# Optimization experiments

Measured on AMD Instinct MI355X. Metric: run time of the kernel, lower is better.

The kernel has to match this reference:

```python
import jax, jax.numpy as jnp
import numpy as np

B, N, M = 128, 256, 1024
EPS = 1e-16
NORM_EPS = 1e-8  # torch cosine_similarity denominator clamp


def setup_inputs() -> dict:
    key = jax.random.key(0)
    ks = jax.random.split(key, 9)
    return {
        "memory": jax.random.normal(ks[0], (B, N, M), jnp.float32),
        "k": jax.random.normal(ks[1], (B, M), jnp.float32),
        "beta": jax.random.uniform(ks[2], (B, 1), jnp.float32),
        "g": jax.random.uniform(ks[3], (B, 1), jnp.float32),
        "s": jax.random.uniform(ks[4], (B, 3), jnp.float32),
        "gamma": jax.random.uniform(ks[5], (B, 1), jnp.float32),
        "w_prev": jax.random.uniform(ks[6], (B, N), jnp.float32),
        "e": jax.random.uniform(ks[7], (B, M), jnp.float32),
        "a": jax.random.normal(ks[8], (B, M), jnp.float32),
    }


def reference(memory, k, beta, g, s, gamma, w_prev, e, a):
    # --- _similarity: cosine similarity + softmax over N rows ---
    mem_e = memory + EPS              # (B, N, M)
    k_e = k + EPS                     # (B, M)
    dot = jnp.einsum("bnm,bm->bn", mem_e, k_e)
    mnorm = jnp.maximum(jnp.linalg.norm(mem_e, axis=-1), NORM_EPS)      # (B, N)
    knorm = jnp.maximum(jnp.linalg.norm(k_e, axis=-1), NORM_EPS)        # (B,)
    cos = dot / (mnorm * knorm[:, None])
    w_c = jax.nn.softmax(beta * cos, axis=-1)                           # (B, N)

    # --- _interpolate with previous weighting ---
    w_g = g * w_c + (1.0 - g) * w_prev                                  # (B, N)

    # --- _shift: circular convolution with 3-tap kernel s ---
    # result[m] = s0*w[m-1] + s1*w[m] + s2*w[m+1]  (circular, matches _convolve)
    w_t = (s[:, 0:1] * jnp.roll(w_g, 1, axis=1)
           + s[:, 1:2] * w_g
           + s[:, 2:3] * jnp.roll(w_g, -1, axis=1))                     # (B, N)

    # --- _sharpen ---
    w_pow = w_t ** gamma
    w = w_pow / (jnp.sum(w_pow, axis=1, keepdims=True) + EPS)           # (B, N)

    # --- write: batched outer-product erase/add (fused, no per-batch loop) ---
    erase = jnp.einsum("bn,bm->bnm", w, e)                              # (B, N, M)
    add = jnp.einsum("bn,bm->bnm", w, a)                                # (B, N, M)
    new_memory = memory * (1.0 - erase) + add

    # --- read ---
    read = jnp.einsum("bn,bnm->bm", w, new_memory)                      # (B, M)

    return read, new_memory, w
```

## Files before the change

kernel.cpp:

```cpp
#include <hip/hip_runtime.h>

#define B_ 128
#define N_ 256
#define M_ 1024
#define EPS_ 1e-16f
#define NORM_EPS_ 1e-8f

#define SPLIT_ 8
#define NSUB_ (N_ / SPLIT_)

typedef float f32x4 __attribute__((ext_vector_type(4)));

__device__ __forceinline__ float wave_reduce_sum(float v) {
#pragma unroll
    for (int off = 32; off; off >>= 1) v += __shfl_xor(v, off, 64);
    return v;
}

__device__ __forceinline__ float wave_reduce_max(float v) {
#pragma unroll
    for (int off = 32; off; off >>= 1) v = fmaxf(v, __shfl_xor(v, off, 64));
    return v;
}

__global__ void sim_kernel(const float* __restrict__ memory,
                           const float* __restrict__ k,
                           float* __restrict__ dot_out,
                           float* __restrict__ mnorm2_out,
                           float* __restrict__ read_out) {
    const int wave = threadIdx.x >> 6;
    const int lane = threadIdx.x & 63;
    const int row  = blockIdx.x * 4 + wave;
    const int b    = row >> 8;

    if (blockIdx.x < (B_ * M_) / 256) {
        read_out[blockIdx.x * 256 + threadIdx.x] = 0.f;
    }

    const f32x4* __restrict__ mrow = (const f32x4*)(memory + (size_t)row * M_);
    const f32x4* __restrict__ krow = (const f32x4*)(k + (size_t)b * M_);

    float dacc = 0.f, nacc = 0.f;
#pragma unroll
    for (int it = 0; it < 4; ++it) {
        const int idx = it * 64 + lane;
        f32x4 mv = mrow[idx];
        f32x4 kv = krow[idx];
        float m0 = mv.x + EPS_, m1 = mv.y + EPS_, m2 = mv.z + EPS_, m3 = mv.w + EPS_;
        float c0 = kv.x + EPS_, c1 = kv.y + EPS_, c2 = kv.z + EPS_, c3 = kv.w + EPS_;
        dacc += m0 * c0 + m1 * c1 + m2 * c2 + m3 * c3;
        nacc += m0 * m0 + m1 * m1 + m2 * m2 + m3 * m3;
    }
    dacc = wave_reduce_sum(dacc);
    nacc = wave_reduce_sum(nacc);
    if (lane == 0) {
        dot_out[row]    = dacc;
        mnorm2_out[row] = nacc;
    }
}

__global__ void fused_weight_write_kernel(const float* __restrict__ memory,
                                          const float* __restrict__ k,
                                          const float* __restrict__ beta,
                                          const float* __restrict__ g,
                                          const float* __restrict__ s,
                                          const float* __restrict__ gamma,
                                          const float* __restrict__ w_prev,
                                          const float* __restrict__ e,
                                          const float* __restrict__ a,
                                          const float* __restrict__ dot_in,
                                          const float* __restrict__ mnorm2_in,
                                          float* __restrict__ w_out,
                                          float* __restrict__ newmem_out,
                                          float* __restrict__ read_out) {
    const int b    = blockIdx.x >> 3;
    const int part = blockIdx.x & (SPLIT_ - 1);
    const int tid  = threadIdx.x;
    const int lane = tid & 63;
    const int wave = tid >> 6;
    const int n    = tid;

    __shared__ float red[4];
    __shared__ float s_wg[N_];

    f32x4 kv = ((const f32x4*)(k + (size_t)b * M_))[tid];
    float k0 = kv.x + EPS_, k1 = kv.y + EPS_, k2 = kv.z + EPS_, k3 = kv.w + EPS_;
    float kk = k0 * k0 + k1 * k1 + k2 * k2 + k3 * k3;
    kk = wave_reduce_sum(kk);
    if (lane == 0) red[wave] = kk;
    __syncthreads();
    const float knorm = fmaxf(sqrtf(red[0] + red[1] + red[2] + red[3]), NORM_EPS_);
    __syncthreads();

    const float mnorm = fmaxf(sqrtf(mnorm2_in[(size_t)b * N_ + n]), NORM_EPS_);
    const float cosv  = dot_in[(size_t)b * N_ + n] / (mnorm * knorm);
    const float x     = beta[b] * cosv;

    float mx = wave_reduce_max(x);
    if (lane == 0) red[wave] = mx;
    __syncthreads();
    mx = fmaxf(fmaxf(red[0], red[1]), fmaxf(red[2], red[3]));
    __syncthreads();
    const float ex = __expf(x - mx);
    float es = wave_reduce_sum(ex);
    if (lane == 0) red[wave] = es;
    __syncthreads();
    es = red[0] + red[1] + red[2] + red[3];
    __syncthreads();
    const float w_c = ex / es;

    const float gb  = g[b];
    const float w_g = gb * w_c + (1.f - gb) * w_prev[(size_t)b * N_ + n];
    s_wg[n] = w_g;
    __syncthreads();

    const float s0 = s[b * 3 + 0], s1 = s[b * 3 + 1], s2 = s[b * 3 + 2];
    const float w_t = s0 * s_wg[(n + N_ - 1) & (N_ - 1)]
                    + s1 * s_wg[n]
                    + s2 * s_wg[(n + 1) & (N_ - 1)];
    __syncthreads();

    const float w_pow = powf(w_t, gamma[b]);
    float ps = wave_reduce_sum(w_pow);
    if (lane == 0) red[wave] = ps;
    __syncthreads();
    ps = red[0] + red[1] + red[2] + red[3];
    const float w_final = w_pow / (ps + EPS_);

    s_wg[n] = w_final;
    if (part == 0) w_out[(size_t)b * N_ + n] = w_final;
    __syncthreads();

    const f32x4 ev = ((const f32x4*)(e + (size_t)b * M_))[tid];
    const f32x4 av = ((const f32x4*)(a + (size_t)b * M_))[tid];

    const size_t base = (size_t)b * N_ * M_;
    f32x4 racc = {0.f, 0.f, 0.f, 0.f};

#pragma unroll 4
    for (int j = 0; j < NSUB_; ++j) {
        const int nn = part * NSUB_ + j;
        const f32x4 mv = ((const f32x4*)(memory + base + (size_t)nn * M_))[tid];
        const float wn = s_wg[part * NSUB_ + j];
        f32x4 nv;
        nv.x = mv.x * (1.f - wn * ev.x) + wn * av.x;
        nv.y = mv.y * (1.f - wn * ev.y) + wn * av.y;
        nv.z = mv.z * (1.f - wn * ev.z) + wn * av.z;
        nv.w = mv.w * (1.f - wn * ev.w) + wn * av.w;
        ((f32x4*)(newmem_out + base + (size_t)nn * M_))[tid] = nv;
        racc.x += wn * nv.x;
        racc.y += wn * nv.y;
        racc.z += wn * nv.z;
        racc.w += wn * nv.w;
    }

    float* rrow = read_out + (size_t)b * M_ + tid * 4;
    atomicAdd(rrow + 0, racc.x);
    atomicAdd(rrow + 1, racc.y);
    atomicAdd(rrow + 2, racc.z);
    atomicAdd(rrow + 3, racc.w);
}

extern "C" void kernel_launch(void* const* d_in, const int* in_sizes, int n_in,
                              void* d_out, int out_size, void* d_ws, size_t ws_size,
                              hipStream_t stream) {
    (void)in_sizes; (void)n_in; (void)out_size; (void)ws_size;

    const float* memory = (const float*)d_in[0];
    const float* k      = (const float*)d_in[1];
    const float* beta   = (const float*)d_in[2];
    const float* g      = (const float*)d_in[3];
    const float* s      = (const float*)d_in[4];
    const float* gamma  = (const float*)d_in[5];
    const float* w_prev = (const float*)d_in[6];
    const float* e      = (const float*)d_in[7];
    const float* a      = (const float*)d_in[8];

    float* out        = (float*)d_out;
    float* read_out   = out;
    float* newmem_out = out + (size_t)B_ * M_;
    float* w_out      = newmem_out + (size_t)B_ * N_ * M_;

    float* ws        = (float*)d_ws;
    float* dot_ws    = ws;
    float* mnorm2_ws = ws + (size_t)B_ * N_;

    sim_kernel<<<(B_ * N_) / 4, 256, 0, stream>>>(memory, k, dot_ws, mnorm2_ws,
                                                  read_out);
    fused_weight_write_kernel<<<B_ * SPLIT_, 256, 0, stream>>>(
        memory, k, beta, g, s, gamma, w_prev, e, a,
        dot_ws, mnorm2_ws, w_out, newmem_out, read_out);
}
```

Measured before the change: 270.9 us.

## Double write-kernel split and batch sixteen rows per similarity block

```diff
diff --git a/kernel.cpp b/kernel.cpp
--- a/kernel.cpp
+++ b/kernel.cpp
@@ -6,8 +6,9 @@
 #define EPS_ 1e-16f
 #define NORM_EPS_ 1e-8f
 
-#define SPLIT_ 8
+#define SPLIT_ 16
 #define NSUB_ (N_ / SPLIT_)
+#define SIMROWS_ 16
 
 typedef float f32x4 __attribute__((ext_vector_type(4)));
 
@@ -30,32 +31,41 @@
                            float* __restrict__ read_out) {
     const int wave = threadIdx.x >> 6;
     const int lane = threadIdx.x & 63;
-    const int row  = blockIdx.x * 4 + wave;
-    const int b    = row >> 8;
-
-    if (blockIdx.x < (B_ * M_) / 256) {
-        read_out[blockIdx.x * 256 + threadIdx.x] = 0.f;
+    const int blk  = blockIdx.x;
+    const int b    = blk >> 4;
+
+    if (blk < (B_ * M_) / 256) {
+        read_out[blk * 256 + threadIdx.x] = 0.f;
     }
 
-    const f32x4* __restrict__ mrow = (const f32x4*)(memory + (size_t)row * M_);
     const f32x4* __restrict__ krow = (const f32x4*)(k + (size_t)b * M_);
-
-    float dacc = 0.f, nacc = 0.f;
+    const f32x4 kv0 = krow[0 * 64 + lane];
+    const f32x4 kv1 = krow[1 * 64 + lane];
+    const f32x4 kv2 = krow[2 * 64 + lane];
+    const f32x4 kv3 = krow[3 * 64 + lane];
+
 #pragma unroll
-    for (int it = 0; it < 4; ++it) {
-        const int idx = it * 64 + lane;
-        f32x4 mv = mrow[idx];
-        f32x4 kv = krow[idx];
-        float m0 = mv.x + EPS_, m1 = mv.y + EPS_, m2 = mv.z + EPS_, m3 = mv.w + EPS_;
-        float c0 = kv.x + EPS_, c1 = kv.y + EPS_, c2 = kv.z + EPS_, c3 = kv.w + EPS_;
-        dacc += m0 * c0 + m1 * c1 + m2 * c2 + m3 * c3;
-        nacc += m0 * m0 + m1 * m1 + m2 * m2 + m3 * m3;
-    }
-    dacc = wave_reduce_sum(dacc);
-    nacc = wave_reduce_sum(nacc);
-    if (lane == 0) {
-        dot_out[row]    = dacc;
-        mnorm2_out[row] = nacc;
+    for (int j = 0; j < 4; ++j) {
+        const int row = blk * SIMROWS_ + wave * 4 + j;
+        const f32x4* __restrict__ mrow = (const f32x4*)(memory + (size_t)row * M_);
+        const f32x4 m0 = mrow[0 * 64 + lane];
+        const f32x4 m1 = mrow[1 * 64 + lane];
+        const f32x4 m2 = mrow[2 * 64 + lane];
+        const f32x4 m3 = mrow[3 * 64 + lane];
+        float dacc = m0.x * kv0.x + m0.y * kv0.y + m0.z * kv0.z + m0.w * kv0.w
+                   + m1.x * kv1.x + m1.y * kv1.y + m1.z * kv1.z + m1.w * kv1.w
+                   + m2.x * kv2.x + m2.y * kv2.y + m2.z * kv2.z + m2.w * kv2.w
+                   + m3.x * kv3.x + m3.y * kv3.y + m3.z * kv3.z + m3.w * kv3.w;
+        float nacc = m0.x * m0.x + m0.y * m0.y + m0.z * m0.z + m0.w * m0.w
+                   + m1.x * m1.x + m1.y * m1.y + m1.z * m1.z + m1.w * m1.w
+                   + m2.x * m2.x + m2.y * m2.y + m2.z * m2.z + m2.w * m2.w
+                   + m3.x * m3.x + m3.y * m3.y + m3.z * m3.z + m3.w * m3.w;
+        dacc = wave_reduce_sum(dacc);
+        nacc = wave_reduce_sum(nacc);
+        if (lane == 0) {
+            dot_out[row]    = dacc;
+            mnorm2_out[row] = nacc;
+        }
     }
 }
 
@@ -73,7 +83,7 @@
                                           float* __restrict__ w_out,
                                           float* __restrict__ newmem_out,
                                           float* __restrict__ read_out) {
-    const int b    = blockIdx.x >> 3;
+    const int b    = blockIdx.x >> 4;
     const int part = blockIdx.x & (SPLIT_ - 1);
     const int tid  = threadIdx.x;
     const int lane = tid & 63;
@@ -83,6 +93,9 @@
     __shared__ float red[4];
     __shared__ float s_wg[N_];
 
+    const f32x4 ev = ((const f32x4*)(e + (size_t)b * M_))[tid];
+    const f32x4 av = ((const f32x4*)(a + (size_t)b * M_))[tid];
+
     f32x4 kv = ((const f32x4*)(k + (size_t)b * M_))[tid];
     float k0 = kv.x + EPS_, k1 = kv.y + EPS_, k2 = kv.z + EPS_, k3 = kv.w + EPS_;
     float kk = k0 * k0 + k1 * k1 + k2 * k2 + k3 * k3;
@@ -131,9 +144,6 @@
     if (part == 0) w_out[(size_t)b * N_ + n] = w_final;
     __syncthreads();
 
-    const f32x4 ev = ((const f32x4*)(e + (size_t)b * M_))[tid];
-    const f32x4 av = ((const f32x4*)(a + (size_t)b * M_))[tid];
-
     const size_t base = (size_t)b * N_ * M_;
     f32x4 racc = {0.f, 0.f, 0.f, 0.f};
 
@@ -141,7 +151,7 @@
     for (int j = 0; j < NSUB_; ++j) {
         const int nn = part * NSUB_ + j;
         const f32x4 mv = ((const f32x4*)(memory + base + (size_t)nn * M_))[tid];
-        const float wn = s_wg[part * NSUB_ + j];
+        const float wn = s_wg[nn];
         f32x4 nv;
         nv.x = mv.x * (1.f - wn * ev.x) + wn * av.x;
         nv.y = mv.y * (1.f - wn * ev.y) + wn * av.y;
@@ -185,8 +195,8 @@
     float* dot_ws    = ws;
     float* mnorm2_ws = ws + (size_t)B_ * N_;
 
-    sim_kernel<<<(B_ * N_) / 4, 256, 0, stream>>>(memory, k, dot_ws, mnorm2_ws,
-                                                  read_out);
+    sim_kernel<<<(B_ * N_) / SIMROWS_, 256, 0, stream>>>(memory, k, dot_ws,
+                                                         mnorm2_ws, read_out);
     fused_weight_write_kernel<<<B_ * SPLIT_, 256, 0, stream>>>(
         memory, k, beta, g, s, gamma, w_prev, e, a,
         dot_ws, mnorm2_ws, w_out, newmem_out, read_out);
```

Measured after the change: 277.4 us. +2.4%, slower.
